# Performance work log

Hardware: AMD Instinct MI355X
Metric: run time of the kernel (lower is better)

Reference implementation:

```python
import jax, jax.numpy as jnp
import numpy as np

B, L, D = 8, 1024, 512
H, DK, DV = 8, 64, 64
EPS = 1e-6
NEG = -1e9


def setup_inputs() -> dict:
    key = jax.random.key(0)
    ks = jax.random.split(key, 12)
    def xavier(k, shape):
        fan_out, fan_in = shape
        bound = float(np.sqrt(6.0 / (fan_in + fan_out)))
        return jax.random.uniform(k, shape, jnp.float32, -bound, bound)
    return {
        "q": jax.random.normal(ks[0], (B, L, D), jnp.float32),
        "k": jax.random.normal(ks[1], (B, L, D), jnp.float32),
        "v": jax.random.normal(ks[2], (B, L, D), jnp.float32),
        "event_type": jax.random.randint(ks[3], (B, L), 0, 2, jnp.int32),
        "mask": jax.random.randint(ks[4], (B, L, L), 0, 2, jnp.int32).astype(bool),
        "w_qs": xavier(ks[5], (H * DK, D)),
        "w_ex_en_qs": xavier(ks[6], (H * DK, D)),
        "w_ks": xavier(ks[7], (H * DK, D)),
        "w_vs": xavier(ks[8], (H * DV, D)),
        "w_fc": xavier(ks[9], (D, H * DV)),
        "b_fc": jnp.zeros((D,), jnp.float32),
        "ln_gamma": jnp.ones((D,), jnp.float32),
        "ln_beta": jnp.zeros((D,), jnp.float32),
    }


def _layer_norm(x, gamma, beta):
    mu = jnp.mean(x, axis=-1, keepdims=True)
    var = jnp.var(x, axis=-1, keepdims=True)
    return (x - mu) * jax.lax.rsqrt(var + EPS) * gamma + beta


def reference(q, k, v, event_type, mask, w_qs, w_ex_en_qs, w_ks, w_vs, w_fc, b_fc, ln_gamma, ln_beta):
    residual = q
    qn = _layer_norm(q, ln_gamma, ln_beta)  # normalize_before=True

    # event-type flags: en_en = prev is en AND present is en; ex_en = prev is ex AND present is en
    is_en = event_type != 0                                   # [B, L]
    en_en = (is_en[:, :, None] & is_en[:, None, :])[:, None]  # [B, 1, L, L]
    ex_en = ((~is_en)[:, :, None] & is_en[:, None, :])[:, None]

    def proj(x, w, d):  # torch Linear: x @ w.T, then split heads -> [B, H, L, d]
        return (x @ w.T).reshape(B, L, H, d).transpose(0, 2, 1, 3)

    q_en = proj(qn, w_qs, DK)
    q_ex = proj(qn, w_ex_en_qs, DK)
    kh = proj(k, w_ks, DK)
    vh = proj(v, w_vs, DV)

    temp = jnp.asarray(DK ** 0.5, qn.dtype)
    scores_en = jnp.einsum('bhqd,bhkd->bhqk', q_en / temp, kh)
    scores_en = jnp.where(mask[:, None], NEG, scores_en)      # masked branch
    scores_ex = jnp.einsum('bhqd,bhkd->bhqk', q_ex / temp, kh)  # unmasked branch

    blended = en_en * scores_en + ex_en * scores_ex           # [B, H, L, L]
    attn = jax.nn.softmax(blended, axis=-1)

    out = jnp.einsum('bhqk,bhkd->bhqd', attn, vh)             # PV
    out = out.transpose(0, 2, 1, 3).reshape(B, L, H * DV)
    out = out @ w_fc.T + b_fc
    out = out + residual
    return out, attn
```

## Files before the change

kernel.cpp:

```cpp
#include <hip/hip_runtime.h>

typedef __attribute__((ext_vector_type(8))) short bf16x8;
typedef __attribute__((ext_vector_type(4))) float f32x4;

#define DEVI static __device__ __forceinline__

constexpr float NEGV = -1e9f;

DEVI unsigned short f2b(float f) {
  union { float f; unsigned int u; } c; c.f = f;
  unsigned int lsb = (c.u >> 16) & 1u;
  return (unsigned short)((c.u + 0x7fffu + lsb) >> 16);
}
DEVI float sb2f(short s) {
  union { unsigned int u; float f; } c;
  c.u = ((unsigned int)(unsigned short)s) << 16;
  return c.f;
}

DEVI void gload16(const unsigned short* g, unsigned short* l) {
  __builtin_amdgcn_global_load_lds(
      (const __attribute__((address_space(1))) unsigned int*)g,
      (__attribute__((address_space(3))) unsigned int*)l, 16, 0, 0);
}

__global__ void mask_detect(const unsigned int* __restrict__ m, int n, int* flag) {
  unsigned int v = 0;
  for (int i = blockIdx.x * blockDim.x + threadIdx.x; i < n; i += gridDim.x * blockDim.x)
    v |= m[i];
  if (v & ~1u) atomicOr(flag, 1);
}

__global__ void mask_canon_bits(const void* __restrict__ mraw, unsigned int* __restrict__ mb,
                                int nwords, const int* __restrict__ flag) {
  int i = blockIdx.x * blockDim.x + threadIdx.x;
  if (i >= nwords) return;
  bool isbytes = (*flag != 0);
  unsigned int out = 0;
  if (isbytes) {
    const unsigned int* p = (const unsigned int*)mraw + (size_t)i * 8;
    #pragma unroll
    for (int w = 0; w < 8; w++) {
      unsigned int bw = p[w];
      out |= ((bw & 1u) << (w * 4)) | (((bw >> 8) & 1u) << (w * 4 + 1)) |
             (((bw >> 16) & 1u) << (w * 4 + 2)) | (((bw >> 24) & 1u) << (w * 4 + 3));
    }
  } else {
    const int4* p = (const int4*)mraw + (size_t)i * 8;
    #pragma unroll
    for (int w = 0; w < 8; w++) {
      int4 v = p[w];
      out |= ((v.x != 0 ? 1u : 0u) << (w * 4)) | ((v.y != 0 ? 1u : 0u) << (w * 4 + 1)) |
             ((v.z != 0 ? 1u : 0u) << (w * 4 + 2)) | ((v.w != 0 ? 1u : 0u) << (w * 4 + 3));
    }
  }
  mb[i] = out;
}

__global__ __launch_bounds__(256) void ln_kernel(const float* __restrict__ q,
    const float* __restrict__ gamma, const float* __restrict__ beta,
    unsigned short* __restrict__ qn) {
  int row = blockIdx.x;
  int t = threadIdx.x;
  const float* x = q + (size_t)row * 512;
  float2 v = reinterpret_cast<const float2*>(x)[t];
  float s = v.x + v.y, s2 = v.x * v.x + v.y * v.y;
  #pragma unroll
  for (int o = 32; o; o >>= 1) { s += __shfl_xor(s, o); s2 += __shfl_xor(s2, o); }
  __shared__ float ls[4], ls2[4];
  int w = t >> 6;
  if ((t & 63) == 0) { ls[w] = s; ls2[w] = s2; }
  __syncthreads();
  float S = ls[0] + ls[1] + ls[2] + ls[3];
  float S2 = ls2[0] + ls2[1] + ls2[2] + ls2[3];
  float mu = S * (1.f / 512.f);
  float var = S2 * (1.f / 512.f) - mu * mu;
  float r = rsqrtf(var + 1e-6f);
  float g0 = gamma[t * 2], g1 = gamma[t * 2 + 1];
  float b0 = beta[t * 2], b1 = beta[t * 2 + 1];
  ushort2 o;
  o.x = f2b((v.x - mu) * r * g0 + b0);
  o.y = f2b((v.y - mu) * r * g1 + b1);
  reinterpret_cast<ushort2*>(qn + (size_t)row * 512)[t] = o;
}

template<int MODE, bool CVX, bool CVW>
__global__ __launch_bounds__(256) void gemm_bt(
    const void* __restrict__ Xv,
    const void* __restrict__ Wv,
    void* __restrict__ Yv,
    float scale,
    const float* __restrict__ bias,
    const float* __restrict__ resid) {
  constexpr int LDT = 40;
  __shared__ __align__(16) unsigned short lA[64 * LDT];
  __shared__ __align__(16) unsigned short lB[64 * LDT];
  int t = threadIdx.x;
  int w = t >> 6, l = t & 63, lr = l & 15, lg = l >> 4;
  int mb = blockIdx.x * 64, nb = blockIdx.y * 64;
  f32x4 acc[4];
  #pragma unroll
  for (int n = 0; n < 4; n++) acc[n] = {0.f, 0.f, 0.f, 0.f};
  int sr = t >> 2, sc = (t & 3) * 8;
  for (int k0 = 0; k0 < 512; k0 += 32) {
    __syncthreads();
    if constexpr (CVX) {
      const float* src = (const float*)Xv + (size_t)(mb + sr) * 512 + k0 + sc;
      float4 x0 = *reinterpret_cast<const float4*>(src);
      float4 x1 = *reinterpret_cast<const float4*>(src + 4);
      ushort4 h0{f2b(x0.x), f2b(x0.y), f2b(x0.z), f2b(x0.w)};
      ushort4 h1{f2b(x1.x), f2b(x1.y), f2b(x1.z), f2b(x1.w)};
      *reinterpret_cast<ushort4*>(&lA[sr * LDT + sc]) = h0;
      *reinterpret_cast<ushort4*>(&lA[sr * LDT + sc + 4]) = h1;
    } else {
      *reinterpret_cast<float4*>(&lA[sr * LDT + sc]) =
          *reinterpret_cast<const float4*>((const unsigned short*)Xv + (size_t)(mb + sr) * 512 + k0 + sc);
    }
    if constexpr (CVW) {
      const float* src = (const float*)Wv + (size_t)(nb + sr) * 512 + k0 + sc;
      float4 x0 = *reinterpret_cast<const float4*>(src);
      float4 x1 = *reinterpret_cast<const float4*>(src + 4);
      ushort4 h0{f2b(x0.x), f2b(x0.y), f2b(x0.z), f2b(x0.w)};
      ushort4 h1{f2b(x1.x), f2b(x1.y), f2b(x1.z), f2b(x1.w)};
      *reinterpret_cast<ushort4*>(&lB[sr * LDT + sc]) = h0;
      *reinterpret_cast<ushort4*>(&lB[sr * LDT + sc + 4]) = h1;
    } else {
      *reinterpret_cast<float4*>(&lB[sr * LDT + sc]) =
          *reinterpret_cast<const float4*>((const unsigned short*)Wv + (size_t)(nb + sr) * 512 + k0 + sc);
    }
    __syncthreads();
    bf16x8 a = *reinterpret_cast<const bf16x8*>(&lA[(w * 16 + lr) * LDT + lg * 8]);
    #pragma unroll
    for (int n = 0; n < 4; n++) {
      bf16x8 bb = *reinterpret_cast<const bf16x8*>(&lB[(n * 16 + lr) * LDT + lg * 8]);
      acc[n] = __builtin_amdgcn_mfma_f32_16x16x32_bf16(a, bb, acc[n], 0, 0, 0);
    }
  }
  #pragma unroll
  for (int n = 0; n < 4; n++) {
    #pragma unroll
    for (int j = 0; j < 4; j++) {
      int m = mb + w * 16 + lg * 4 + j;
      int c = nb + n * 16 + lr;
      float val = acc[n][j] * scale;
      if constexpr (MODE == 0) {
        reinterpret_cast<unsigned short*>(Yv)[(size_t)m * 512 + c] = f2b(val);
      } else if constexpr (MODE == 1) {
        int bb_ = m >> 10, ll = m & 1023, hh = c >> 6, dd = c & 63;
        reinterpret_cast<unsigned short*>(Yv)[((size_t)((bb_ * 8 + hh) * 64 + dd)) * 1024 + ll] = f2b(val);
      } else {
        reinterpret_cast<float*>(Yv)[(size_t)m * 512 + c] =
            val + bias[c] + resid[(size_t)m * 512 + c];
      }
    }
  }
}

__global__ __launch_bounds__(256) void attn_kernel(
    const unsigned short* __restrict__ qen,
    const unsigned short* __restrict__ qex,
    const unsigned short* __restrict__ kh,
    const unsigned short* __restrict__ vhT,
    const int* __restrict__ etype,
    const unsigned int* __restrict__ mbits,
    float* __restrict__ attn_g,
    unsigned short* __restrict__ pv_out) {
  int lid = blockIdx.x;
  int xcd = lid & 7, slot = lid >> 3;
  int qt = slot & 15;
  int g = ((slot >> 4) << 3) | xcd;
  int h = g & 7, b = g >> 3;

  int t = threadIdx.x, w = t >> 6, l = t & 63, lr = l & 15, lg = l >> 4;
  __shared__ unsigned int ekbits[32];
  __shared__ unsigned int mkill[64 * 33];
  __shared__ __align__(16) unsigned short klds[2][2048];
  __shared__ __align__(16) unsigned short vlds[2][2048];
  __shared__ __align__(16) unsigned short pbuf[4][16][40];

  int qb = qt * 64 + w * 16;
  int qrowA = qb + lr;
  bool evA = etype[b * 1024 + qrowA] != 0;
  const unsigned short* qp = evA ? qen : qex;
  size_t qoff = (size_t)(b * 1024 + qrowA) * 512 + h * 64;
  bf16x8 a0 = *reinterpret_cast<const bf16x8*>(qp + qoff + lg * 8);
  bf16x8 a1 = *reinterpret_cast<const bf16x8*>(qp + qoff + 32 + lg * 8);

  if (t < 32) {
    unsigned int wdd = 0;
    const int4* ep = (const int4*)(etype + b * 1024 + t * 32);
    #pragma unroll
    for (int j4 = 0; j4 < 8; j4++) {
      int4 e = ep[j4];
      wdd |= ((e.x != 0 ? 1u : 0u) << (j4 * 4)) | ((e.y != 0 ? 1u : 0u) << (j4 * 4 + 1)) |
             ((e.z != 0 ? 1u : 0u) << (j4 * 4 + 2)) | ((e.w != 0 ? 1u : 0u) << (j4 * 4 + 3));
    }
    ekbits[t] = wdd;
  }
  {
    const unsigned int* mslice = mbits + ((size_t)(b * 1024 + qt * 64)) * 32;
    for (int i = t; i < 2048; i += 256) {
      int row = i >> 5, wd = i & 31;
      bool evq_row = etype[b * 1024 + qt * 64 + row] != 0;
      mkill[row * 33 + wd] = evq_row ? mslice[i] : 0u;
    }
  }

  int qrc[4], qlc[4];
  #pragma unroll
  for (int j = 0; j < 4; j++) { qlc[j] = w * 16 + lg * 4 + j; qrc[j] = qt * 64 + qlc[j]; }

  int srow = t >> 3, sb8 = t & 7;
  const unsigned short* kgsrc = kh + ((size_t)(b * 1024) + srow) * 512 + h * 64
                                + ((sb8 ^ (srow & 7)) << 3);
  unsigned short* kdst0 = &klds[0][(t & 192) * 8];
  unsigned short* kdst1 = &klds[1][(t & 192) * 8];
  int vrow = t >> 2, vb4 = t & 3;
  const unsigned short* vb_base = vhT + ((size_t)((b * 8 + h) * 64)) * 1024;
  const unsigned short* vgsrc = vb_base + (size_t)vrow * 1024 + ((vb4 ^ ((vrow >> 1) & 3)) << 3);
  unsigned short* vdst0 = &vlds[0][(t & 192) * 8];
  unsigned short* vdst1 = &vlds[1][(t & 192) * 8];

  gload16(kgsrc, kdst0);
  __syncthreads();

  float srun[4] = {0.f, 0.f, 0.f, 0.f};
  for (int c = 0; c < 32; c++) {
    int cur = c & 1;
    if (c < 31) gload16(kgsrc + (size_t)(c + 1) * 32 * 512, cur ? kdst0 : kdst1);
    #pragma unroll
    for (int c2 = 0; c2 < 2; c2++) {
      int kt = c * 2 + c2;
      int row = c2 * 16 + lr, r7 = row & 7;
      bf16x8 b0 = *reinterpret_cast<const bf16x8*>(&klds[cur][row * 64 + ((lg ^ r7) << 3)]);
      bf16x8 b1 = *reinterpret_cast<const bf16x8*>(&klds[cur][row * 64 + (((4 + lg) ^ r7) << 3)]);
      f32x4 cc = {0.f, 0.f, 0.f, 0.f};
      cc = __builtin_amdgcn_mfma_f32_16x16x32_bf16(a0, b0, cc, 0, 0, 0);
      cc = __builtin_amdgcn_mfma_f32_16x16x32_bf16(a1, b1, cc, 0, 0, 0);
      int wcol = kt >> 1, bitpos = ((kt & 1) << 4) + lr;
      bool ekb = (ekbits[wcol] >> bitpos) & 1;
      #pragma unroll
      for (int j = 0; j < 4; j++) {
        bool mk = (mkill[qlc[j] * 33 + wcol] >> bitpos) & 1;
        float val = ekb ? (mk ? NEGV : cc[j]) : 0.f;
        srun[j] += __expf(val);
      }
    }
    __syncthreads();
  }
  float rS[4];
  #pragma unroll
  for (int j = 0; j < 4; j++) {
    float s = srun[j];
    s += __shfl_xor(s, 1); s += __shfl_xor(s, 2);
    s += __shfl_xor(s, 4); s += __shfl_xor(s, 8);
    rS[j] = 1.f / s;
  }

  f32x4 oacc[4];
  #pragma unroll
  for (int n = 0; n < 4; n++) oacc[n] = {0.f, 0.f, 0.f, 0.f};
  float* ag = attn_g + ((size_t)(b * 8 + h)) * 1024 * 1024;
  float* agrow = ag + (size_t)(qb + lr) * 1024 + lg * 8;

  gload16(kgsrc, kdst0);
  gload16(vgsrc, vdst0);
  __syncthreads();

  for (int c = 0; c < 32; c++) {
    int cur = c & 1;
    if (c < 31) {
      gload16(kgsrc + (size_t)(c + 1) * 32 * 512, cur ? kdst0 : kdst1);
      gload16(vgsrc + (size_t)(c + 1) * 32, cur ? vdst0 : vdst1);
    }
    #pragma unroll
    for (int c2 = 0; c2 < 2; c2++) {
      int kt = c * 2 + c2;
      int row = c2 * 16 + lr, r7 = row & 7;
      bf16x8 b0 = *reinterpret_cast<const bf16x8*>(&klds[cur][row * 64 + ((lg ^ r7) << 3)]);
      bf16x8 b1 = *reinterpret_cast<const bf16x8*>(&klds[cur][row * 64 + (((4 + lg) ^ r7) << 3)]);
      f32x4 cc = {0.f, 0.f, 0.f, 0.f};
      cc = __builtin_amdgcn_mfma_f32_16x16x32_bf16(a0, b0, cc, 0, 0, 0);
      cc = __builtin_amdgcn_mfma_f32_16x16x32_bf16(a1, b1, cc, 0, 0, 0);
      int wcol = kt >> 1, bitpos = ((kt & 1) << 4) + lr;
      bool ekb = (ekbits[wcol] >> bitpos) & 1;
      #pragma unroll
      for (int j = 0; j < 4; j++) {
        bool mk = (mkill[qlc[j] * 33 + wcol] >> bitpos) & 1;
        float val = ekb ? (mk ? NEGV : cc[j]) : 0.f;
        float p = __expf(val) * rS[j];
        pbuf[w][lg * 4 + j][(c2 << 4) + lr] = f2b(p);
      }
      if (c2) {
        bf16x8 pa = *reinterpret_cast<const bf16x8*>(&pbuf[w][lr][lg * 8]);
        f32x4 f0, f1;
        f0[0] = sb2f(pa[0]); f0[1] = sb2f(pa[1]); f0[2] = sb2f(pa[2]); f0[3] = sb2f(pa[3]);
        f1[0] = sb2f(pa[4]); f1[1] = sb2f(pa[5]); f1[2] = sb2f(pa[6]); f1[3] = sb2f(pa[7]);
        __builtin_nontemporal_store(f0, reinterpret_cast<f32x4*>(agrow + c * 32));
        __builtin_nontemporal_store(f1, reinterpret_cast<f32x4*>(agrow + c * 32 + 4));
        #pragma unroll
        for (int n = 0; n < 4; n++) {
          int vr = n * 16 + lr;
          int cb = (lg ^ ((vr >> 1) & 3)) << 3;
          bf16x8 vb = *reinterpret_cast<const bf16x8*>(&vlds[cur][vr * 32 + cb]);
          oacc[n] = __builtin_amdgcn_mfma_f32_16x16x32_bf16(pa, vb, oacc[n], 0, 0, 0);
        }
      }
    }
    __syncthreads();
  }
  #pragma unroll
  for (int n = 0; n < 4; n++) {
    #pragma unroll
    for (int j = 0; j < 4; j++) {
      __builtin_nontemporal_store(f2b(oacc[n][j]),
          &pv_out[(size_t)(b * 1024 + qrc[j]) * 512 + h * 64 + n * 16 + lr]);
    }
  }
}

extern "C" void kernel_launch(void* const* d_in, const int* in_sizes, int n_in,
                              void* d_out, int out_size, void* d_ws, size_t ws_size,
                              hipStream_t stream) {
  (void)in_sizes; (void)n_in; (void)out_size; (void)ws_size;
  const float* q     = (const float*)d_in[0];
  const float* k     = (const float*)d_in[1];
  const float* v     = (const float*)d_in[2];
  const int* etype   = (const int*)d_in[3];
  const void* mask_raw = d_in[4];
  const float* w_qs  = (const float*)d_in[5];
  const float* w_ex  = (const float*)d_in[6];
  const float* w_ks  = (const float*)d_in[7];
  const float* w_vs  = (const float*)d_in[8];
  const float* w_fc  = (const float*)d_in[9];
  const float* b_fc  = (const float*)d_in[10];
  const float* gamma = (const float*)d_in[11];
  const float* beta  = (const float*)d_in[12];

  char* ws = (char*)d_ws;
  const size_t MB = 1024 * 1024;
  unsigned short* qn   = (unsigned short*)(ws);
  unsigned short* qen  = (unsigned short*)(ws + 8 * MB);
  unsigned short* qex  = (unsigned short*)(ws + 16 * MB);
  unsigned short* khb  = (unsigned short*)(ws + 24 * MB);
  unsigned short* vhT  = (unsigned short*)(ws + 32 * MB);
  unsigned short* ao   = (unsigned short*)(ws + 40 * MB);
  unsigned int* mbits  = (unsigned int*)(ws + 48 * MB);
  int* mflag           = (int*)(ws + 49 * MB);

  float* outp = (float*)d_out;
  float* attn_g = outp + (size_t)8 * 1024 * 512;

  ln_kernel<<<8192, 256, 0, stream>>>(q, gamma, beta, qn);

  const int MASK_N = 8 * 1024 * 1024;
  hipMemsetAsync(mflag, 0, 4, stream);
  mask_detect<<<2048, 256, 0, stream>>>((const unsigned int*)mask_raw, MASK_N / 4, mflag);
  const int NWORDS = MASK_N / 32;
  mask_canon_bits<<<(NWORDS + 255) / 256, 256, 0, stream>>>(mask_raw, mbits, NWORDS, mflag);

  dim3 gg(128, 8);
  gemm_bt<0, false, true><<<gg, 256, 0, stream>>>(qn, w_qs, qen, 0.125f, nullptr, nullptr);
  gemm_bt<0, false, true><<<gg, 256, 0, stream>>>(qn, w_ex, qex, 0.125f, nullptr, nullptr);
  gemm_bt<0, true,  true><<<gg, 256, 0, stream>>>(k,  w_ks, khb, 1.0f, nullptr, nullptr);
  gemm_bt<1, true,  true><<<gg, 256, 0, stream>>>(v,  w_vs, vhT, 1.0f, nullptr, nullptr);

  attn_kernel<<<dim3(1024), 256, 0, stream>>>(qen, qex, khb, vhT, etype, mbits,
                                              attn_g, ao);

  gemm_bt<2, false, true><<<gg, 256, 0, stream>>>(ao, w_fc, outp, 1.0f, b_fc, q);
}
```

Before: 277.2 us.

## Load K and V fragments directly from global memory instead of LDS staging

Removes the double-buffered LDS staging of K and V tiles (global_load_lds with per-chunk __syncthreads) and has each wave read its MFMA operand fragments straight from global memory. The four waves in a block then read the same K/V data redundantly, relying on L1/L2 caching rather than shared memory. The intent is to drop the barriers and LDS traffic, at the cost of more global load instructions and latency that the loop unrolling has to hide.

Result: slower. 318.0 us (+14.7%).

```diff
diff --git a/kernel.cpp b/kernel.cpp
--- a/kernel.cpp
+++ b/kernel.cpp
@@ -16,12 +16,6 @@
   union { unsigned int u; float f; } c;
   c.u = ((unsigned int)(unsigned short)s) << 16;
   return c.f;
-}
-
-DEVI void gload16(const unsigned short* g, unsigned short* l) {
-  __builtin_amdgcn_global_load_lds(
-      (const __attribute__((address_space(1))) unsigned int*)g,
-      (__attribute__((address_space(3))) unsigned int*)l, 16, 0, 0);
 }
 
 __global__ void mask_detect(const unsigned int* __restrict__ m, int n, int* flag) {
@@ -174,8 +168,6 @@
   int t = threadIdx.x, w = t >> 6, l = t & 63, lr = l & 15, lg = l >> 4;
   __shared__ unsigned int ekbits[32];
   __shared__ unsigned int mkill[64 * 33];
-  __shared__ __align__(16) unsigned short klds[2][2048];
-  __shared__ __align__(16) unsigned short vlds[2][2048];
   __shared__ __align__(16) unsigned short pbuf[4][16][40];
 
   int qb = qt * 64 + w * 16;
@@ -205,48 +197,32 @@
       mkill[row * 33 + wd] = evq_row ? mslice[i] : 0u;
     }
   }
+  __syncthreads();
 
   int qrc[4], qlc[4];
   #pragma unroll
   for (int j = 0; j < 4; j++) { qlc[j] = w * 16 + lg * 4 + j; qrc[j] = qt * 64 + qlc[j]; }
 
-  int srow = t >> 3, sb8 = t & 7;
-  const unsigned short* kgsrc = kh + ((size_t)(b * 1024) + srow) * 512 + h * 64
-                                + ((sb8 ^ (srow & 7)) << 3);
-  unsigned short* kdst0 = &klds[0][(t & 192) * 8];
-  unsigned short* kdst1 = &klds[1][(t & 192) * 8];
-  int vrow = t >> 2, vb4 = t & 3;
-  const unsigned short* vb_base = vhT + ((size_t)((b * 8 + h) * 64)) * 1024;
-  const unsigned short* vgsrc = vb_base + (size_t)vrow * 1024 + ((vb4 ^ ((vrow >> 1) & 3)) << 3);
-  unsigned short* vdst0 = &vlds[0][(t & 192) * 8];
-  unsigned short* vdst1 = &vlds[1][(t & 192) * 8];
-
-  gload16(kgsrc, kdst0);
-  __syncthreads();
+  const unsigned short* kptr = kh + ((size_t)b * 1024 + lr) * 512 + h * 64 + lg * 8;
+  const unsigned short* vptr = vhT + ((size_t)((b * 8 + h) * 64) + lr) * 1024 + lg * 8;
 
   float srun[4] = {0.f, 0.f, 0.f, 0.f};
-  for (int c = 0; c < 32; c++) {
-    int cur = c & 1;
-    if (c < 31) gload16(kgsrc + (size_t)(c + 1) * 32 * 512, cur ? kdst0 : kdst1);
-    #pragma unroll
-    for (int c2 = 0; c2 < 2; c2++) {
-      int kt = c * 2 + c2;
-      int row = c2 * 16 + lr, r7 = row & 7;
-      bf16x8 b0 = *reinterpret_cast<const bf16x8*>(&klds[cur][row * 64 + ((lg ^ r7) << 3)]);
-      bf16x8 b1 = *reinterpret_cast<const bf16x8*>(&klds[cur][row * 64 + (((4 + lg) ^ r7) << 3)]);
-      f32x4 cc = {0.f, 0.f, 0.f, 0.f};
-      cc = __builtin_amdgcn_mfma_f32_16x16x32_bf16(a0, b0, cc, 0, 0, 0);
-      cc = __builtin_amdgcn_mfma_f32_16x16x32_bf16(a1, b1, cc, 0, 0, 0);
-      int wcol = kt >> 1, bitpos = ((kt & 1) << 4) + lr;
-      bool ekb = (ekbits[wcol] >> bitpos) & 1;
-      #pragma unroll
-      for (int j = 0; j < 4; j++) {
-        bool mk = (mkill[qlc[j] * 33 + wcol] >> bitpos) & 1;
-        float val = ekb ? (mk ? NEGV : cc[j]) : 0.f;
-        srun[j] += __expf(val);
-      }
-    }
-    __syncthreads();
+  #pragma unroll 4
+  for (int kt = 0; kt < 64; kt++) {
+    const unsigned short* kp = kptr + (size_t)kt * 16 * 512;
+    bf16x8 b0 = *reinterpret_cast<const bf16x8*>(kp);
+    bf16x8 b1 = *reinterpret_cast<const bf16x8*>(kp + 32);
+    f32x4 cc = {0.f, 0.f, 0.f, 0.f};
+    cc = __builtin_amdgcn_mfma_f32_16x16x32_bf16(a0, b0, cc, 0, 0, 0);
+    cc = __builtin_amdgcn_mfma_f32_16x16x32_bf16(a1, b1, cc, 0, 0, 0);
+    int wcol = kt >> 1, bitpos = ((kt & 1) << 4) + lr;
+    bool ekb = (ekbits[wcol] >> bitpos) & 1;
+    #pragma unroll
+    for (int j = 0; j < 4; j++) {
+      bool mk = (mkill[qlc[j] * 33 + wcol] >> bitpos) & 1;
+      float val = ekb ? (mk ? NEGV : cc[j]) : 0.f;
+      srun[j] += __expf(val);
+    }
   }
   float rS[4];
   #pragma unroll
@@ -263,51 +239,38 @@
   float* ag = attn_g + ((size_t)(b * 8 + h)) * 1024 * 1024;
   float* agrow = ag + (size_t)(qb + lr) * 1024 + lg * 8;
 
-  gload16(kgsrc, kdst0);
-  gload16(vgsrc, vdst0);
-  __syncthreads();
-
-  for (int c = 0; c < 32; c++) {
-    int cur = c & 1;
-    if (c < 31) {
-      gload16(kgsrc + (size_t)(c + 1) * 32 * 512, cur ? kdst0 : kdst1);
-      gload16(vgsrc + (size_t)(c + 1) * 32, cur ? vdst0 : vdst1);
-    }
-    #pragma unroll
-    for (int c2 = 0; c2 < 2; c2++) {
-      int kt = c * 2 + c2;
-      int row = c2 * 16 + lr, r7 = row & 7;
-      bf16x8 b0 = *reinterpret_cast<const bf16x8*>(&klds[cur][row * 64 + ((lg ^ r7) << 3)]);
-      bf16x8 b1 = *reinterpret_cast<const bf16x8*>(&klds[cur][row * 64 + (((4 + lg) ^ r7) << 3)]);
-      f32x4 cc = {0.f, 0.f, 0.f, 0.f};
-      cc = __builtin_amdgcn_mfma_f32_16x16x32_bf16(a0, b0, cc, 0, 0, 0);
-      cc = __builtin_amdgcn_mfma_f32_16x16x32_bf16(a1, b1, cc, 0, 0, 0);
-      int wcol = kt >> 1, bitpos = ((kt & 1) << 4) + lr;
-      bool ekb = (ekbits[wcol] >> bitpos) & 1;
+  #pragma unroll 2
+  for (int kt = 0; kt < 64; kt++) {
+    const unsigned short* kp = kptr + (size_t)kt * 16 * 512;
+    bf16x8 b0 = *reinterpret_cast<const bf16x8*>(kp);
+    bf16x8 b1 = *reinterpret_cast<const bf16x8*>(kp + 32);
+    f32x4 cc = {0.f, 0.f, 0.f, 0.f};
+    cc = __builtin_amdgcn_mfma_f32_16x16x32_bf16(a0, b0, cc, 0, 0, 0);
+    cc = __builtin_amdgcn_mfma_f32_16x16x32_bf16(a1, b1, cc, 0, 0, 0);
+    int wcol = kt >> 1, bitpos = ((kt & 1) << 4) + lr;
+    bool ekb = (ekbits[wcol] >> bitpos) & 1;
+    #pragma unroll
+    for (int j = 0; j < 4; j++) {
+      bool mk = (mkill[qlc[j] * 33 + wcol] >> bitpos) & 1;
+      float val = ekb ? (mk ? NEGV : cc[j]) : 0.f;
+      float p = __expf(val) * rS[j];
+      pbuf[w][lg * 4 + j][((kt & 1) << 4) + lr] = f2b(p);
+    }
+    if (kt & 1) {
+      int kc = kt >> 1;
+      bf16x8 pa = *reinterpret_cast<const bf16x8*>(&pbuf[w][lr][lg * 8]);
+      f32x4 f0, f1;
+      f0[0] = sb2f(pa[0]); f0[1] = sb2f(pa[1]); f0[2] = sb2f(pa[2]); f0[3] = sb2f(pa[3]);
+      f1[0] = sb2f(pa[4]); f1[1] = sb2f(pa[5]); f1[2] = sb2f(pa[6]); f1[3] = sb2f(pa[7]);
+      __builtin_nontemporal_store(f0, reinterpret_cast<f32x4*>(agrow + kc * 32));
+      __builtin_nontemporal_store(f1, reinterpret_cast<f32x4*>(agrow + kc * 32 + 4));
       #pragma unroll
-      for (int j = 0; j < 4; j++) {
-        bool mk = (mkill[qlc[j] * 33 + wcol] >> bitpos) & 1;
-        float val = ekb ? (mk ? NEGV : cc[j]) : 0.f;
-        float p = __expf(val) * rS[j];
-        pbuf[w][lg * 4 + j][(c2 << 4) + lr] = f2b(p);
+      for (int n = 0; n < 4; n++) {
+        const unsigned short* vp = vptr + (size_t)n * 16 * 1024 + kc * 32;
+        bf16x8 vb = *reinterpret_cast<const bf16x8*>(vp);
+        oacc[n] = __builtin_amdgcn_mfma_f32_16x16x32_bf16(pa, vb, oacc[n], 0, 0, 0);
       }
-      if (c2) {
-        bf16x8 pa = *reinterpret_cast<const bf16x8*>(&pbuf[w][lr][lg * 8]);
-        f32x4 f0, f1;
-        f0[0] = sb2f(pa[0]); f0[1] = sb2f(pa[1]); f0[2] = sb2f(pa[2]); f0[3] = sb2f(pa[3]);
-        f1[0] = sb2f(pa[4]); f1[1] = sb2f(pa[5]); f1[2] = sb2f(pa[6]); f1[3] = sb2f(pa[7]);
-        __builtin_nontemporal_store(f0, reinterpret_cast<f32x4*>(agrow + c * 32));
-        __builtin_nontemporal_store(f1, reinterpret_cast<f32x4*>(agrow + c * 32 + 4));
-        #pragma unroll
-        for (int n = 0; n < 4; n++) {
-          int vr = n * 16 + lr;
-          int cb = (lg ^ ((vr >> 1) & 3)) << 3;
-          bf16x8 vb = *reinterpret_cast<const bf16x8*>(&vlds[cur][vr * 32 + cb]);
-          oacc[n] = __builtin_amdgcn_mfma_f32_16x16x32_bf16(pa, vb, oacc[n], 0, 0, 0);
-        }
-      }
-    }
-    __syncthreads();
+    }
   }
   #pragma unroll
   for (int n = 0; n < 4; n++) {
```
